# Kernel optimization log

Hardware: AMD Instinct MI355X
Metric: run time of the kernel (lower is better)

Reference implementation:

```python
import jax, jax.numpy as jnp
import numpy as np

N_QUBITS = 8

# Quantum circuit math: starting from |0...0>, apply RX(x_i) then RY(theta_i) on each
# wire independently (product state preserved). Exact PauliZ expectation per wire:
#   RX(x)|0> = cos(x/2)|0> - i sin(x/2)|1>;  after RY(t):
#   <Z> = cos(x) * cos(t)
# This is the exact closed form of the full state-vector simulation the torch module runs.

def setup_inputs() -> dict:
    key = jax.random.key(0)
    k1, k2, k3, k4 = jax.random.split(key, 4)
    B, S, D, F = 4, 4096, 1024, 4096
    x = jax.random.normal(k1, (B, S, D), dtype=jnp.float32)
    theta = jax.random.normal(k2, (N_QUBITS,), dtype=jnp.float32)
    W1 = jax.random.normal(k3, (F, N_QUBITS), dtype=jnp.float32) * (1.0 / np.sqrt(N_QUBITS))
    W2 = jax.random.normal(k4, (D, F), dtype=jnp.float32) * (1.0 / np.sqrt(F))
    return {"x": x, "theta": theta, "W1": W1, "W2": W2}


def reference(x, theta, W1, W2):
    # Encoder only reads the first n_qubits features of each token.
    z = jnp.cos(x[..., :N_QUBITS]) * jnp.cos(theta)          # [B, S, Q] PauliZ expectations
    h = jax.nn.relu(jnp.einsum('bsq,fq->bsf', z, W1))        # [B, S, ffn_dim]
    return jnp.einsum('bsf,df->bsd', h, W2)                  # [B, S, embed_dim]
```

## Files before the change

kernel.cpp:

```cpp
#include <hip/hip_runtime.h>
#include <hip/hip_bf16.h>
#include <math.h>


using f32x4  = __attribute__((ext_vector_type(4))) float;
using bf16x8 = __attribute__((ext_vector_type(8))) short;
using i32x4  = __attribute__((ext_vector_type(4))) int;

#define M_TOT 16384
#define N_TOT 1024
#define K_TOT 4096
#define NKT   128
#define TILEB 16384

static const size_t H_BYTES   = (size_t)M_TOT * K_TOT * 2;
static const size_t W2B_BYTES = (size_t)N_TOT * K_TOT * 2;
static const size_t WS_NEED   = H_BYTES + W2B_BYTES;

#define SWZ32(row, bytecol) ((bytecol) ^ ((((row) >> 1) & 3) << 4))

#define GLD16(gp, lp) __builtin_amdgcn_global_load_lds( \
    (const __attribute__((address_space(1))) unsigned int*)(const void*)(gp), \
    (__attribute__((address_space(3))) unsigned int*)(void*)(lp), 16, 0, 0)

static __device__ inline unsigned short f2bf(float f) {
    __hip_bfloat16 b = __float2bfloat16(f);
    unsigned short u;
    __builtin_memcpy(&u, &b, 2);
    return u;
}

__global__ __launch_bounds__(256)
void k_prep(const float* __restrict__ x, const float* __restrict__ theta,
            const float* __restrict__ W1, const float* __restrict__ W2,
            char* __restrict__ hws, char* __restrict__ w2ws)
{
    __shared__ float sZ[256 * 8];
    __shared__ float sW[128 * 8];
    const int tid = threadIdx.x;

    if (blockIdx.x < 2048) {
        const int bx = blockIdx.x >> 5;
        const int by = blockIdx.x & 31;

        {
            const float* xp = x + ((size_t)bx * 256 + tid) * 1024;
            f32x4 a = *reinterpret_cast<const f32x4*>(xp);
            f32x4 b = *reinterpret_cast<const f32x4*>(xp + 4);
            #pragma unroll
            for (int q = 0; q < 4; ++q) {
                sZ[tid * 8 + q]     = cosf(a[q]) * cosf(theta[q]);
                sZ[tid * 8 + 4 + q] = cosf(b[q]) * cosf(theta[q + 4]);
            }
        }
        *reinterpret_cast<f32x4*>(&sW[tid * 4]) =
            *reinterpret_cast<const f32x4*>(W1 + (size_t)by * 1024 + tid * 4);
        __syncthreads();

        const int tm = tid >> 4;
        const int tk = tid & 15;

        f32x4 wA[8], wB[8];
        #pragma unroll
        for (int kk = 0; kk < 8; ++kk) {
            wA[kk] = *reinterpret_cast<const f32x4*>(&sW[(tk * 8 + kk) * 8]);
            wB[kk] = *reinterpret_cast<const f32x4*>(&sW[(tk * 8 + kk) * 8 + 4]);
        }

        const int kt    = by * 4 + (tk >> 2);
        const int slotb = (tk & 3) * 16;
        char* tb = hws + ((size_t)bx * NKT + kt) * TILEB;

        #pragma unroll
        for (int i = 0; i < 16; ++i) {
            const int row = tm * 16 + i;
            f32x4 za = *reinterpret_cast<const f32x4*>(&sZ[row * 8]);
            f32x4 zb = *reinterpret_cast<const f32x4*>(&sZ[row * 8 + 4]);
            unsigned hu[8];
            #pragma unroll
            for (int kk = 0; kk < 8; ++kk) {
                float h = 0.f;
                #pragma unroll
                for (int q = 0; q < 4; ++q) {
                    h = fmaf(za[q], wA[kk][q], h);
                    h = fmaf(zb[q], wB[kk][q], h);
                }
                hu[kk] = (unsigned)f2bf(fmaxf(h, 0.f));
            }
            i32x4 pk;
            pk[0] = (int)(hu[0] | (hu[1] << 16));
            pk[1] = (int)(hu[2] | (hu[3] << 16));
            pk[2] = (int)(hu[4] | (hu[5] << 16));
            pk[3] = (int)(hu[6] | (hu[7] << 16));
            *reinterpret_cast<i32x4*>(tb + row * 64 + SWZ32(row, slotb)) = pk;
        }
    } else {
        const int gt = (blockIdx.x - 2048) * 256 + tid;
        const int n  = gt >> 9;
        const int k8 = gt & 511;
        const float* p = W2 + (size_t)n * K_TOT + k8 * 8;
        f32x4 a = *reinterpret_cast<const f32x4*>(p);
        f32x4 b = *reinterpret_cast<const f32x4*>(p + 4);
        i32x4 pk;
        pk[0] = (int)((unsigned)f2bf(a[0]) | ((unsigned)f2bf(a[1]) << 16));
        pk[1] = (int)((unsigned)f2bf(a[2]) | ((unsigned)f2bf(a[3]) << 16));
        pk[2] = (int)((unsigned)f2bf(b[0]) | ((unsigned)f2bf(b[1]) << 16));
        pk[3] = (int)((unsigned)f2bf(b[2]) | ((unsigned)f2bf(b[3]) << 16));
        const int nt = n >> 8, row = n & 255, kt = k8 >> 2, slotb = (k8 & 3) * 16;
        char* dst = w2ws + ((size_t)nt * NKT + kt) * TILEB + row * 64 + SWZ32(row, slotb);
        *reinterpret_cast<i32x4*>(dst) = pk;
    }
}


#define DS_FRAGS(RD, BUF1) do {                                                   \
    const char* sa_ = ldsA + (BUF1) * 16384;                                      \
    const char* sb_ = ldsB + (BUF1) * 16384;                                      \
    _Pragma("unroll")                                                             \
    for (int i = 0; i < 8; ++i)                                                   \
        Pa[RD][i] = *reinterpret_cast<const bf16x8*>(sa_ + aoff + i * 1024);      \
    _Pragma("unroll")                                                             \
    for (int j = 0; j < 4; ++j)                                                   \
        Pb[RD][j] = *reinterpret_cast<const bf16x8*>(sb_ + boff + j * 1024);      \
} while (0)

#define STAGE4(KT3, BUF3) do {                                                    \
    const char* ga_ = aT + (size_t)(KT3) * TILEB;                                 \
    const char* gb_ = bT + (size_t)(KT3) * TILEB;                                 \
    GLD16(ga_ + gofs,        ldsA + (BUF3) * 16384 + lofs);                       \
    GLD16(ga_ + 8192 + gofs, ldsA + (BUF3) * 16384 + 8192 + lofs);                \
    GLD16(gb_ + gofs,        ldsB + (BUF3) * 16384 + lofs);                       \
    GLD16(gb_ + 8192 + gofs, ldsB + (BUF3) * 16384 + 8192 + lofs);                \
} while (0)

#define MFMA32(USE) do {                                                          \
    __builtin_amdgcn_s_setprio(1);                                                \
    _Pragma("unroll")                                                             \
    for (int i = 0; i < 8; ++i)                                                   \
        _Pragma("unroll")                                                         \
        for (int j = 0; j < 4; ++j)                                               \
            acc[i][j] = __builtin_amdgcn_mfma_f32_16x16x32_bf16(Pa[USE][i], Pb[USE][j], acc[i][j], 0, 0, 0); \
    __builtin_amdgcn_s_setprio(0);                                                \
} while (0)

#define PHASE(BUF, KT, WN, DOREAD, DOSTAGE) do {                                  \
    asm volatile("s_waitcnt vmcnt(" #WN ")" ::: "memory");                        \
    __builtin_amdgcn_sched_barrier(0);                                            \
    __builtin_amdgcn_s_barrier();                                                 \
    __builtin_amdgcn_sched_barrier(0);                                            \
    if (DOREAD)  DS_FRAGS(((BUF) + 1) & 1, ((BUF) + 1) & 3);                      \
    if (DOSTAGE) STAGE4((KT) + 3, ((BUF) + 3) & 3);                               \
    __builtin_amdgcn_sched_barrier(0);                                            \
    MFMA32((BUF) & 1);                                                            \
} while (0)

__global__ __launch_bounds__(512, 2)
void k_gemm(const char* __restrict__ hws, const char* __restrict__ w2ws,
            float* __restrict__ out)
{
    __shared__ __align__(16) char lds[131072];
    char* const ldsA = lds;
    char* const ldsB = lds + 65536;

    const int tid  = threadIdx.x;
    const int lane = tid & 63;
    const int wave = tid >> 6;
    const int wm = wave >> 2;
    const int wn = wave & 3;
    const int mt = blockIdx.x;
    const int nt = blockIdx.y;

    const char* aT = hws  + (size_t)mt * NKT * TILEB;
    const char* bT = w2ws + (size_t)nt * NKT * TILEB;

    const int l16 = lane & 15;
    const int lkb = (lane >> 4) * 16;
    const int arow0 = wm * 128 + l16;
    const int aoff  = arow0 * 64 + SWZ32(arow0, lkb);
    const int brow0 = wn * 64 + l16;
    const int boff  = brow0 * 64 + SWZ32(brow0, lkb);

    const int gofs = tid * 16;
    const int lofs = wave * 1024;

    bf16x8 Pa[2][8];
    bf16x8 Pb[2][4];

    f32x4 acc[8][4];
    #pragma unroll
    for (int i = 0; i < 8; ++i)
        #pragma unroll
        for (int j = 0; j < 4; ++j)
            acc[i][j] = {0.f, 0.f, 0.f, 0.f};

    STAGE4(0, 0);
    STAGE4(1, 1);
    STAGE4(2, 2);
    asm volatile("s_waitcnt vmcnt(8)" ::: "memory");
    __builtin_amdgcn_sched_barrier(0);
    __builtin_amdgcn_s_barrier();
    __builtin_amdgcn_sched_barrier(0);
    DS_FRAGS(0, 0);

    #pragma unroll 1
    for (int t = 0; t < 124; t += 4) {
        PHASE(0, t,     4, 1, 1);
        PHASE(1, t + 1, 4, 1, 1);
        PHASE(2, t + 2, 4, 1, 1);
        PHASE(3, t + 3, 4, 1, 1);
    }
    PHASE(0, 124, 4, 1, 1);
    PHASE(1, 125, 4, 1, 0);
    PHASE(2, 126, 0, 1, 0);
    MFMA32(1);

    const int orow0 = mt * 256 + wm * 128 + (lane >> 4) * 4;
    const int ocol0 = nt * 256 + wn * 64 + l16;
    #pragma unroll
    for (int i = 0; i < 8; ++i)
        #pragma unroll
        for (int j = 0; j < 4; ++j)
            #pragma unroll
            for (int jj = 0; jj < 4; ++jj)
                out[(size_t)(orow0 + i * 16 + jj) * N_TOT + (ocol0 + j * 16)] = acc[i][j][jj];
}

__global__ __launch_bounds__(256, 3)
void qffn_fused(const float* __restrict__ x, const float* __restrict__ theta,
                const float* __restrict__ W1, const float* __restrict__ W2,
                float* __restrict__ out)
{
    __shared__ __align__(16) unsigned short sA[128 * 64];
    __shared__ __align__(16) unsigned short sB[128 * 64];

    const int tid  = threadIdx.x;
    const int lane = tid & 63;
    const int wave = tid >> 6;
    const int m0 = blockIdx.x * 128;
    const int n0 = blockIdx.y * 128;

    const int arow = tid & 127;
    float zc[8];
    {
        const float* xp = x + (size_t)(m0 + arow) * 1024;
        f32x4 x0 = *reinterpret_cast<const f32x4*>(xp);
        f32x4 x1 = *reinterpret_cast<const f32x4*>(xp + 4);
        #pragma unroll
        for (int q = 0; q < 4; ++q) {
            zc[q]     = cosf(x0[q]) * cosf(theta[q]);
            zc[q + 4] = cosf(x1[q]) * cosf(theta[q + 4]);
        }
    }

    f32x4 acc[4][4];
    #pragma unroll
    for (int i = 0; i < 4; ++i)
        #pragma unroll
        for (int j = 0; j < 4; ++j)
            acc[i][j] = {0.f, 0.f, 0.f, 0.f};

    const int wr  = (wave >> 1) * 64;
    const int wc  = (wave & 1) * 64;
    const int l16 = lane & 15;
    const int lk8 = (lane >> 4) * 8;

    for (int k0 = 0; k0 < K_TOT; k0 += 64) {
        #pragma unroll
        for (int g = 0; g < 4; ++g) {
            const int cg  = (tid >> 7) + 2 * g;
            const int cgu = __builtin_amdgcn_readfirstlane(cg);
            const float* w1p = W1 + (size_t)(k0 + cgu * 8) * 8;
            i32x4 pk;
            #pragma unroll
            for (int p = 0; p < 4; ++p) {
                float h0 = 0.f, h1 = 0.f;
                #pragma unroll
                for (int q = 0; q < 8; ++q) {
                    h0 = fmaf(zc[q], w1p[(2 * p) * 8 + q], h0);
                    h1 = fmaf(zc[q], w1p[(2 * p + 1) * 8 + q], h1);
                }
                pk[p] = (int)(((unsigned)f2bf(fmaxf(h0, 0.f))) |
                              (((unsigned)f2bf(fmaxf(h1, 0.f))) << 16));
            }
            const int off = (arow * 64 + cg * 8) ^ ((arow & 7) << 3);
            *reinterpret_cast<i32x4*>(&sA[off]) = pk;
        }
        {
            const int fi = tid & 15;
            const int rb = tid >> 4;
            #pragma unroll
            for (int r = 0; r < 8; ++r) {
                const int row = rb + r * 16;
                f32x4 v = *(reinterpret_cast<const f32x4*>(W2 + (size_t)(n0 + row) * K_TOT + k0) + fi);
                unsigned p0 = (unsigned)f2bf(v[0]) | ((unsigned)f2bf(v[1]) << 16);
                unsigned p1 = (unsigned)f2bf(v[2]) | ((unsigned)f2bf(v[3]) << 16);
                const int off = (row * 64 + fi * 4) ^ ((row & 7) << 3);
                *reinterpret_cast<unsigned*>(&sB[off])     = p0;
                *reinterpret_cast<unsigned*>(&sB[off + 2]) = p1;
            }
        }
        __syncthreads();

        #pragma unroll
        for (int s = 0; s < 2; ++s) {
            bf16x8 af[4], bfr[4];
            #pragma unroll
            for (int i = 0; i < 4; ++i) {
                const int row = wr + i * 16 + l16;
                const int off = (row * 64 + s * 32 + lk8) ^ ((row & 7) << 3);
                af[i] = *reinterpret_cast<const bf16x8*>(&sA[off]);
            }
            #pragma unroll
            for (int j = 0; j < 4; ++j) {
                const int row = wc + j * 16 + l16;
                const int off = (row * 64 + s * 32 + lk8) ^ ((row & 7) << 3);
                bfr[j] = *reinterpret_cast<const bf16x8*>(&sB[off]);
            }
            #pragma unroll
            for (int i = 0; i < 4; ++i)
                #pragma unroll
                for (int j = 0; j < 4; ++j)
                    acc[i][j] = __builtin_amdgcn_mfma_f32_16x16x32_bf16(af[i], bfr[j], acc[i][j], 0, 0, 0);
        }
        __syncthreads();
    }

    const int orow0 = m0 + wr + (lane >> 4) * 4;
    const int ocol0 = n0 + wc + l16;
    #pragma unroll
    for (int i = 0; i < 4; ++i)
        #pragma unroll
        for (int j = 0; j < 4; ++j)
            #pragma unroll
            for (int jj = 0; jj < 4; ++jj)
                out[(size_t)(orow0 + i * 16 + jj) * N_TOT + (ocol0 + j * 16)] = acc[i][j][jj];
}

extern "C" void kernel_launch(void* const* d_in, const int* in_sizes, int n_in,
                              void* d_out, int out_size, void* d_ws, size_t ws_size,
                              hipStream_t stream) {
    const float* x     = (const float*)d_in[0];
    const float* theta = (const float*)d_in[1];
    const float* W1    = (const float*)d_in[2];
    const float* W2    = (const float*)d_in[3];
    float* out = (float*)d_out;

    if (ws_size >= WS_NEED) {
        char* hws  = (char*)d_ws;
        char* w2ws = (char*)d_ws + H_BYTES;

        k_prep<<<dim3(4096), dim3(256), 0, stream>>>(x, theta, W1, W2, hws, w2ws);
        k_gemm<<<dim3(M_TOT / 256, N_TOT / 256), dim3(512), 0, stream>>>(hws, w2ws, out);
    } else {
        qffn_fused<<<dim3(M_TOT / 128, N_TOT / 128), dim3(256), 0, stream>>>(x, theta, W1, W2, out);
    }
}
```

Before: 146.5 us.

## Load GEMM B operand directly from global into registers, bypassing LDS

The W2 (B) operand tiles are no longer staged through shared memory. Each wave now loads its B fragments straight from the pre-laid-out global workspace into registers one k-tile ahead, and the W2 prep drops the LDS swizzle to match. LDS use halves to 64 KB, only A is double-staged, and the vmcnt thresholds are adjusted for the new load mix. The aim is to cut LDS traffic and capacity pressure, possibly allowing two blocks per CU. The cost is duplicated global/L2 reads of B across waves and more exposed global-load latency on the register path.

```diff
diff --git a/kernel.cpp b/kernel.cpp
--- a/kernel.cpp
+++ b/kernel.cpp
@@ -107,7 +107,7 @@
         pk[2] = (int)((unsigned)f2bf(b[0]) | ((unsigned)f2bf(b[1]) << 16));
         pk[3] = (int)((unsigned)f2bf(b[2]) | ((unsigned)f2bf(b[3]) << 16));
         const int nt = n >> 8, row = n & 255, kt = k8 >> 2, slotb = (k8 & 3) * 16;
-        char* dst = w2ws + ((size_t)nt * NKT + kt) * TILEB + row * 64 + SWZ32(row, slotb);
+        char* dst = w2ws + ((size_t)nt * NKT + kt) * TILEB + row * 64 + slotb;
         *reinterpret_cast<i32x4*>(dst) = pk;
     }
 }
@@ -115,22 +115,22 @@
 
 #define DS_FRAGS(RD, BUF1) do {                                                   \
     const char* sa_ = ldsA + (BUF1) * 16384;                                      \
-    const char* sb_ = ldsB + (BUF1) * 16384;                                      \
     _Pragma("unroll")                                                             \
     for (int i = 0; i < 8; ++i)                                                   \
         Pa[RD][i] = *reinterpret_cast<const bf16x8*>(sa_ + aoff + i * 1024);      \
+} while (0)
+
+#define B_LOAD(RD, KT1) do {                                                      \
+    const char* gb_ = bT + (size_t)(KT1) * TILEB + bofsG;                         \
     _Pragma("unroll")                                                             \
     for (int j = 0; j < 4; ++j)                                                   \
-        Pb[RD][j] = *reinterpret_cast<const bf16x8*>(sb_ + boff + j * 1024);      \
-} while (0)
-
-#define STAGE4(KT3, BUF3) do {                                                    \
+        Pb[RD][j] = *reinterpret_cast<const bf16x8*>(gb_ + j * 1024);             \
+} while (0)
+
+#define STAGE2(KT3, BUF3) do {                                                    \
     const char* ga_ = aT + (size_t)(KT3) * TILEB;                                 \
-    const char* gb_ = bT + (size_t)(KT3) * TILEB;                                 \
     GLD16(ga_ + gofs,        ldsA + (BUF3) * 16384 + lofs);                       \
     GLD16(ga_ + 8192 + gofs, ldsA + (BUF3) * 16384 + 8192 + lofs);                \
-    GLD16(gb_ + gofs,        ldsB + (BUF3) * 16384 + lofs);                       \
-    GLD16(gb_ + 8192 + gofs, ldsB + (BUF3) * 16384 + 8192 + lofs);                \
 } while (0)
 
 #define MFMA32(USE) do {                                                          \
@@ -143,13 +143,14 @@
     __builtin_amdgcn_s_setprio(0);                                                \
 } while (0)
 
-#define PHASE(BUF, KT, WN, DOREAD, DOSTAGE) do {                                  \
+#define PHASE(BUF, KT, WN, DOB, DOSTAGE) do {                                     \
     asm volatile("s_waitcnt vmcnt(" #WN ")" ::: "memory");                        \
     __builtin_amdgcn_sched_barrier(0);                                            \
     __builtin_amdgcn_s_barrier();                                                 \
     __builtin_amdgcn_sched_barrier(0);                                            \
-    if (DOREAD)  DS_FRAGS(((BUF) + 1) & 1, ((BUF) + 1) & 3);                      \
-    if (DOSTAGE) STAGE4((KT) + 3, ((BUF) + 3) & 3);                               \
+    DS_FRAGS(((BUF) + 1) & 1, ((BUF) + 1) & 3);                                   \
+    if (DOB)     B_LOAD(((BUF) + 1) & 1, (KT) + 1);                               \
+    if (DOSTAGE) STAGE2((KT) + 3, ((BUF) + 3) & 3);                               \
     __builtin_amdgcn_sched_barrier(0);                                            \
     MFMA32((BUF) & 1);                                                            \
 } while (0)
@@ -158,9 +159,7 @@
 void k_gemm(const char* __restrict__ hws, const char* __restrict__ w2ws,
             float* __restrict__ out)
 {
-    __shared__ __align__(16) char lds[131072];
-    char* const ldsA = lds;
-    char* const ldsB = lds + 65536;
+    __shared__ __align__(16) char ldsA[65536];
 
     const int tid  = threadIdx.x;
     const int lane = tid & 63;
@@ -177,8 +176,7 @@
     const int lkb = (lane >> 4) * 16;
     const int arow0 = wm * 128 + l16;
     const int aoff  = arow0 * 64 + SWZ32(arow0, lkb);
-    const int brow0 = wn * 64 + l16;
-    const int boff  = brow0 * 64 + SWZ32(brow0, lkb);
+    const int bofsG = wn * 4096 + l16 * 64 + (lane >> 4) * 16;
 
     const int gofs = tid * 16;
     const int lofs = wave * 1024;
@@ -193,9 +191,10 @@
         for (int j = 0; j < 4; ++j)
             acc[i][j] = {0.f, 0.f, 0.f, 0.f};
 
-    STAGE4(0, 0);
-    STAGE4(1, 1);
-    STAGE4(2, 2);
+    STAGE2(0, 0);
+    STAGE2(1, 1);
+    STAGE2(2, 2);
+    B_LOAD(0, 0);
     asm volatile("s_waitcnt vmcnt(8)" ::: "memory");
     __builtin_amdgcn_sched_barrier(0);
     __builtin_amdgcn_s_barrier();
@@ -204,14 +203,15 @@
 
     #pragma unroll 1
     for (int t = 0; t < 124; t += 4) {
-        PHASE(0, t,     4, 1, 1);
-        PHASE(1, t + 1, 4, 1, 1);
-        PHASE(2, t + 2, 4, 1, 1);
-        PHASE(3, t + 3, 4, 1, 1);
-    }
-    PHASE(0, 124, 4, 1, 1);
-    PHASE(1, 125, 4, 1, 0);
-    PHASE(2, 126, 0, 1, 0);
+        PHASE(0, t,     6, 1, 1);
+        PHASE(1, t + 1, 6, 1, 1);
+        PHASE(2, t + 2, 6, 1, 1);
+        PHASE(3, t + 3, 6, 1, 1);
+    }
+    PHASE(0, 124, 6, 1, 1);
+    PHASE(1, 125, 6, 1, 0);
+    PHASE(2, 126, 4, 1, 0);
+    __builtin_amdgcn_sched_barrier(0);
     MFMA32(1);
 
     const int orow0 = mt * 256 + wm * 128 + (lane >> 4) * 4;
```

Result: slower. 162.8 us (+11.1%).

## Restructure GEMM to K=64 tiles with 8-phase half-tile staged pipeline

Applied to the files above, without the earlier changes.

Changes the workspace layout from 32-element-K tiles to 64-element-K half-tiles (128 rows x 128 bytes) with a wider XOR swizzle, and rewrites the GEMM main loop as an 8-phase schedule. Each phase reads small A fragments and occasionally B fragments, then issues one half-tile async global-to-LDS load. The goal is to cut barrier and wait overhead per unit of K and to interleave loads with MFMA work more finely. In exchange, occupancy drops to one block per CU, each phase carries two barriers, and the hand-scheduled waitcnt logic is fragile.

```diff
diff --git a/kernel.cpp b/kernel.cpp
--- a/kernel.cpp
+++ b/kernel.cpp
@@ -10,14 +10,14 @@
 #define M_TOT 16384
 #define N_TOT 1024
 #define K_TOT 4096
-#define NKT   128
-#define TILEB 16384
+#define NKT   64
+#define HTB   16384
 
 static const size_t H_BYTES   = (size_t)M_TOT * K_TOT * 2;
 static const size_t W2B_BYTES = (size_t)N_TOT * K_TOT * 2;
 static const size_t WS_NEED   = H_BYTES + W2B_BYTES;
 
-#define SWZ32(row, bytecol) ((bytecol) ^ ((((row) >> 1) & 3) << 4))
+#define SWZ(row, bytecol) ((bytecol) ^ (((row) & 7) << 4))
 
 #define GLD16(gp, lp) __builtin_amdgcn_global_load_lds( \
     (const __attribute__((address_space(1))) unsigned int*)(const void*)(gp), \
@@ -67,15 +67,14 @@
             wB[kk] = *reinterpret_cast<const f32x4*>(&sW[(tk * 8 + kk) * 8 + 4]);
         }
 
-        const int kt    = by * 4 + (tk >> 2);
-        const int slotb = (tk & 3) * 16;
-        char* tb = hws + ((size_t)bx * NKT + kt) * TILEB;
+        const int kt    = by * 2 + (tk >> 3);
+        const int slotb = (tk & 7) * 16;
 
         #pragma unroll
         for (int i = 0; i < 16; ++i) {
-            const int row = tm * 16 + i;
-            f32x4 za = *reinterpret_cast<const f32x4*>(&sZ[row * 8]);
-            f32x4 zb = *reinterpret_cast<const f32x4*>(&sZ[row * 8 + 4]);
+            const int R = tm * 16 + i;
+            f32x4 za = *reinterpret_cast<const f32x4*>(&sZ[R * 8]);
+            f32x4 zb = *reinterpret_cast<const f32x4*>(&sZ[R * 8 + 4]);
             unsigned hu[8];
             #pragma unroll
             for (int kk = 0; kk < 8; ++kk) {
@@ -92,7 +91,9 @@
             pk[1] = (int)(hu[2] | (hu[3] << 16));
             pk[2] = (int)(hu[4] | (hu[5] << 16));
             pk[3] = (int)(hu[6] | (hu[7] << 16));
-            *reinterpret_cast<i32x4*>(tb + row * 64 + SWZ32(row, slotb)) = pk;
+            char* dst = hws + ((size_t)((bx * NKT + kt) * 2 + (R >> 7))) * HTB
+                      + (size_t)(R & 127) * 128 + SWZ(R, slotb);
+            *reinterpret_cast<i32x4*>(dst) = pk;
         }
     } else {
         const int gt = (blockIdx.x - 2048) * 256 + tid;
@@ -106,61 +107,66 @@
         pk[1] = (int)((unsigned)f2bf(a[2]) | ((unsigned)f2bf(a[3]) << 16));
         pk[2] = (int)((unsigned)f2bf(b[0]) | ((unsigned)f2bf(b[1]) << 16));
         pk[3] = (int)((unsigned)f2bf(b[2]) | ((unsigned)f2bf(b[3]) << 16));
-        const int nt = n >> 8, row = n & 255, kt = k8 >> 2, slotb = (k8 & 3) * 16;
-        char* dst = w2ws + ((size_t)nt * NKT + kt) * TILEB + row * 64 + SWZ32(row, slotb);
+        const int nt = n >> 8, R = n & 255, kt = k8 >> 3, slotb = (k8 & 7) * 16;
+        char* dst = w2ws + ((size_t)((nt * NKT + kt) * 2 + (R >> 7))) * HTB
+                  + (size_t)(R & 127) * 128 + SWZ(R, slotb);
         *reinterpret_cast<i32x4*>(dst) = pk;
     }
 }
 
 
-#define DS_FRAGS(RD, BUF1) do {                                                   \
-    const char* sa_ = ldsA + (BUF1) * 16384;                                      \
-    const char* sb_ = ldsB + (BUF1) * 16384;                                      \
-    _Pragma("unroll")                                                             \
-    for (int i = 0; i < 8; ++i)                                                   \
-        Pa[RD][i] = *reinterpret_cast<const bf16x8*>(sa_ + aoff + i * 1024);      \
-    _Pragma("unroll")                                                             \
-    for (int j = 0; j < 4; ++j)                                                   \
-        Pb[RD][j] = *reinterpret_cast<const bf16x8*>(sb_ + boff + j * 1024);      \
+#define AHT(KT, H) (aT + ((size_t)(KT) * 2 + (H)) * HTB)
+#define BHT(KT, H) (bT + ((size_t)(KT) * 2 + (H)) * HTB)
+
+#define ST(GP, LO) do {                                                      \
+    const char* g_ = (GP);                                                   \
+    GLD16(g_ + tid * 16,        lds + (LO) + tid * 16);                      \
+    GLD16(g_ + 8192 + tid * 16, lds + (LO) + 8192 + tid * 16);               \
 } while (0)
 
-#define STAGE4(KT3, BUF3) do {                                                    \
-    const char* ga_ = aT + (size_t)(KT3) * TILEB;                                 \
-    const char* gb_ = bT + (size_t)(KT3) * TILEB;                                 \
-    GLD16(ga_ + gofs,        ldsA + (BUF3) * 16384 + lofs);                       \
-    GLD16(ga_ + 8192 + gofs, ldsA + (BUF3) * 16384 + 8192 + lofs);                \
-    GLD16(gb_ + gofs,        ldsB + (BUF3) * 16384 + lofs);                       \
-    GLD16(gb_ + 8192 + gofs, ldsB + (BUF3) * 16384 + 8192 + lofs);                \
+#define VM4 asm volatile("s_waitcnt vmcnt(4)" ::: "memory")
+#define VM0 asm volatile("s_waitcnt vmcnt(0)" ::: "memory")
+#define NOPS ((void)0)
+
+#define PHASE(D, MB, BPH, STG, GATE) do {                                     \
+    const char* ab_ = lds + (D) * 65536 + wm * 16384 + row128;                \
+    bf16x8 a00 = *reinterpret_cast<const bf16x8*>(ab_ + (MB) * 2048 + cs0);   \
+    bf16x8 a01 = *reinterpret_cast<const bf16x8*>(ab_ + (MB) * 2048 + cs1);   \
+    bf16x8 a10 = *reinterpret_cast<const bf16x8*>(ab_ + ((MB)+1) * 2048 + cs0);\
+    bf16x8 a11 = *reinterpret_cast<const bf16x8*>(ab_ + ((MB)+1) * 2048 + cs1);\
+    if (BPH) {                                                                \
+        const char* bb_ = lds + (D) * 65536 + 32768 + bsel + row128;          \
+        _Pragma("unroll")                                                     \
+        for (int j = 0; j < 4; ++j) {                                         \
+            Pb0[j] = *reinterpret_cast<const bf16x8*>(bb_ + j * 2048 + cs0);  \
+            Pb1[j] = *reinterpret_cast<const bf16x8*>(bb_ + j * 2048 + cs1);  \
+        }                                                                     \
+    }                                                                         \
+    STG;                                                                      \
+    if (BPH) asm volatile("s_waitcnt lgkmcnt(8)" ::: "memory");               \
+    __builtin_amdgcn_sched_barrier(0);                                        \
+    __builtin_amdgcn_s_barrier();                                             \
+    asm volatile("s_waitcnt lgkmcnt(0)" ::: "memory");                        \
+    __builtin_amdgcn_sched_barrier(0);                                        \
+    __builtin_amdgcn_s_setprio(1);                                            \
+    _Pragma("unroll")                                                         \
+    for (int j = 0; j < 4; ++j) {                                             \
+        acc[MB][j]     = __builtin_amdgcn_mfma_f32_16x16x32_bf16(a00, Pb0[j], acc[MB][j], 0, 0, 0);     \
+        acc[MB][j]     = __builtin_amdgcn_mfma_f32_16x16x32_bf16(a01, Pb1[j], acc[MB][j], 0, 0, 0);     \
+        acc[(MB)+1][j] = __builtin_amdgcn_mfma_f32_16x16x32_bf16(a10, Pb0[j], acc[(MB)+1][j], 0, 0, 0); \
+        acc[(MB)+1][j] = __builtin_amdgcn_mfma_f32_16x16x32_bf16(a11, Pb1[j], acc[(MB)+1][j], 0, 0, 0); \
+    }                                                                         \
+    __builtin_amdgcn_s_setprio(0);                                            \
+    GATE;                                                                     \
+    __builtin_amdgcn_sched_barrier(0);                                        \
+    __builtin_amdgcn_s_barrier();                                             \
 } while (0)
 
-#define MFMA32(USE) do {                                                          \
-    __builtin_amdgcn_s_setprio(1);                                                \
-    _Pragma("unroll")                                                             \
-    for (int i = 0; i < 8; ++i)                                                   \
-        _Pragma("unroll")                                                         \
-        for (int j = 0; j < 4; ++j)                                               \
-            acc[i][j] = __builtin_amdgcn_mfma_f32_16x16x32_bf16(Pa[USE][i], Pb[USE][j], acc[i][j], 0, 0, 0); \
-    __builtin_amdgcn_s_setprio(0);                                                \
-} while (0)
-
-#define PHASE(BUF, KT, WN, DOREAD, DOSTAGE) do {                                  \
-    asm volatile("s_waitcnt vmcnt(" #WN ")" ::: "memory");                        \
-    __builtin_amdgcn_sched_barrier(0);                                            \
-    __builtin_amdgcn_s_barrier();                                                 \
-    __builtin_amdgcn_sched_barrier(0);                                            \
-    if (DOREAD)  DS_FRAGS(((BUF) + 1) & 1, ((BUF) + 1) & 3);                      \
-    if (DOSTAGE) STAGE4((KT) + 3, ((BUF) + 3) & 3);                               \
-    __builtin_amdgcn_sched_barrier(0);                                            \
-    MFMA32((BUF) & 1);                                                            \
-} while (0)
-
-__global__ __launch_bounds__(512, 2)
+__global__ __launch_bounds__(512, 1)
 void k_gemm(const char* __restrict__ hws, const char* __restrict__ w2ws,
             float* __restrict__ out)
 {
     __shared__ __align__(16) char lds[131072];
-    char* const ldsA = lds;
-    char* const ldsB = lds + 65536;
 
     const int tid  = threadIdx.x;
     const int lane = tid & 63;
@@ -170,22 +176,16 @@
     const int mt = blockIdx.x;
     const int nt = blockIdx.y;
 
-    const char* aT = hws  + (size_t)mt * NKT * TILEB;
-    const char* bT = w2ws + (size_t)nt * NKT * TILEB;
-
-    const int l16 = lane & 15;
-    const int lkb = (lane >> 4) * 16;
-    const int arow0 = wm * 128 + l16;
-    const int aoff  = arow0 * 64 + SWZ32(arow0, lkb);
-    const int brow0 = wn * 64 + l16;
-    const int boff  = brow0 * 64 + SWZ32(brow0, lkb);
-
-    const int gofs = tid * 16;
-    const int lofs = wave * 1024;
-
-    bf16x8 Pa[2][8];
-    bf16x8 Pb[2][4];
-
+    const char* aT = hws  + (size_t)mt * NKT * 2 * HTB;
+    const char* bT = w2ws + (size_t)nt * NKT * 2 * HTB;
+
+    const int l16    = lane & 15;
+    const int row128 = l16 * 128;
+    const int cs0    = ((lane >> 4) * 16) ^ ((l16 & 7) << 4);
+    const int cs1    = cs0 ^ 64;
+    const int bsel   = (wn >> 1) * 16384 + (wn & 1) * 8192;
+
+    bf16x8 Pb0[4], Pb1[4];
     f32x4 acc[8][4];
     #pragma unroll
     for (int i = 0; i < 8; ++i)
@@ -193,26 +193,37 @@
         for (int j = 0; j < 4; ++j)
             acc[i][j] = {0.f, 0.f, 0.f, 0.f};
 
-    STAGE4(0, 0);
-    STAGE4(1, 1);
-    STAGE4(2, 2);
-    asm volatile("s_waitcnt vmcnt(8)" ::: "memory");
+    ST(AHT(0, 0), 0);
+    ST(AHT(0, 1), 16384);
+    ST(BHT(0, 0), 32768);
+    ST(BHT(0, 1), 49152);
+    ST(BHT(1, 0), 98304);
+    ST(BHT(1, 1), 114688);
+    VM4;
     __builtin_amdgcn_sched_barrier(0);
     __builtin_amdgcn_s_barrier();
     __builtin_amdgcn_sched_barrier(0);
-    DS_FRAGS(0, 0);
 
     #pragma unroll 1
-    for (int t = 0; t < 124; t += 4) {
-        PHASE(0, t,     4, 1, 1);
-        PHASE(1, t + 1, 4, 1, 1);
-        PHASE(2, t + 2, 4, 1, 1);
-        PHASE(3, t + 3, 4, 1, 1);
-    }
-    PHASE(0, 124, 4, 1, 1);
-    PHASE(1, 125, 4, 1, 0);
-    PHASE(2, 126, 0, 1, 0);
-    MFMA32(1);
+    for (int it = 0; it < 31; ++it) {
+        const int t = 2 * it;
+        PHASE(0, 0, 1, ST(AHT(t + 1, 0), 65536),         NOPS);
+        PHASE(0, 2, 0, ST(AHT(t + 1, 1), 81920),         NOPS);
+        PHASE(0, 4, 0, ST(BHT(t + 2, 0), 32768),         NOPS);
+        PHASE(0, 6, 0, ST(BHT(t + 2, 1), 49152),         VM4);
+        PHASE(1, 0, 1, ST(AHT(t + 2, 0), 0),             NOPS);
+        PHASE(1, 2, 0, ST(AHT(t + 2, 1), 16384),         NOPS);
+        PHASE(1, 4, 0, ST(BHT(t + 3, 0), 98304),         NOPS);
+        PHASE(1, 6, 0, ST(BHT(t + 3, 1), 114688),        VM4);
+    }
+    PHASE(0, 0, 1, ST(AHT(63, 0), 65536),  NOPS);
+    PHASE(0, 2, 0, ST(AHT(63, 1), 81920),  NOPS);
+    PHASE(0, 4, 0, NOPS,                   NOPS);
+    PHASE(0, 6, 0, NOPS,                   VM0);
+    PHASE(1, 0, 1, NOPS, NOPS);
+    PHASE(1, 2, 0, NOPS, NOPS);
+    PHASE(1, 4, 0, NOPS, NOPS);
+    PHASE(1, 6, 0, NOPS, NOPS);
 
     const int orow0 = mt * 256 + wm * 128 + (lane >> 4) * 4;
     const int ocol0 = nt * 256 + wn * 64 + l16;
```

After: 140.5 us. 4.0% less time.
